# Kernel optimization log

Measured on AMD Instinct MI355X. Metric: run time of the kernel, lower is better.

The kernel has to match this reference:

```python
import jax, jax.numpy as jnp
import numpy as np

D, NH, DH, DM = 1024, 16, 64, 4096
B, S = 2, 2048
EPS = 1e-5


def _layernorm(x, w, b):
    mu = jnp.mean(x, axis=-1, keepdims=True)
    var = jnp.mean((x - mu) ** 2, axis=-1, keepdims=True)
    return (x - mu) * jax.lax.rsqrt(var + EPS) * w + b


def setup_inputs() -> dict:
    key = jax.random.key(0)
    ks = jax.random.split(key, 8)
    scale = D ** (-0.5)
    x = jax.random.normal(ks[0], (B, S, D), dtype=jnp.float32)
    WQ = jax.random.normal(ks[1], (NH, D, DH), dtype=jnp.float32) * scale
    WK = jax.random.normal(ks[2], (NH, D, DH), dtype=jnp.float32) * scale
    WV = jax.random.normal(ks[3], (NH, D, DH), dtype=jnp.float32) * scale
    WO = jax.random.normal(ks[4], (NH, DH, D), dtype=jnp.float32) * scale
    # MLP: torch Linear default init ~ U(-1/sqrt(fan_in), 1/sqrt(fan_in)); stored as [in, out]
    W1 = jax.random.uniform(ks[5], (D, DM), dtype=jnp.float32, minval=-1.0, maxval=1.0) * D ** (-0.5)
    b1 = jnp.zeros((DM,), dtype=jnp.float32)
    W2 = jax.random.uniform(ks[6], (DM, D), dtype=jnp.float32, minval=-1.0, maxval=1.0) * DM ** (-0.5)
    b2 = jnp.zeros((D,), dtype=jnp.float32)
    ln1_w = jnp.ones((D,), dtype=jnp.float32)
    ln1_b = jnp.zeros((D,), dtype=jnp.float32)
    ln2_w = jnp.ones((D,), dtype=jnp.float32)
    ln2_b = jnp.zeros((D,), dtype=jnp.float32)
    return {"x": x, "WQ": WQ, "WK": WK, "WV": WV, "WO": WO,
            "W1": W1, "b1": b1, "W2": W2, "b2": b2,
            "ln1_w": ln1_w, "ln1_b": ln1_b, "ln2_w": ln2_w, "ln2_b": ln2_b}


def reference(x, WQ, WK, WV, WO, W1, b1, W2, b2, ln1_w, ln1_b, ln2_w, ln2_b):
    s = x.shape[1]
    dh = WQ.shape[-1]
    r = x
    h = _layernorm(x, ln1_w, ln1_b)
    # batched across all heads (original loops over h; math identical)
    Q = jnp.einsum('bsd,hde->bhse', h, WQ)
    K = jnp.einsum('bsd,hde->bhse', h, WK)
    V = jnp.einsum('bsd,hde->bhse', h, WV)
    scores = jnp.einsum('bhqe,bhke->bhqk', Q, K) / jnp.sqrt(jnp.float32(dh))
    causal = jnp.tril(jnp.ones((s, s), dtype=bool))  # True = keep
    scores = jnp.where(causal, scores, -jnp.inf)
    attn = jax.nn.softmax(scores, axis=-1)
    ctx = jnp.einsum('bhqk,bhke->bhqe', attn, V)
    ao = jnp.einsum('bhqe,hed->bqd', ctx, WO)  # sum over heads
    x = r + ao
    h2 = _layernorm(x, ln2_w, ln2_b)
    mlp = jax.nn.gelu(h2 @ W1 + b1, approximate=False) @ W2 + b2
    return x + mlp
```

## Files before the change

### kernel.cpp

```cpp
#include <hip/hip_runtime.h>
#include <hip/hip_bf16.h>
#include <cstdint>

#define D_MODEL 1024
#define NHEADS 16
#define DHEAD 64
#define DMLP 4096
#define BATCH 2
#define SEQ 2048
#define ROWS (BATCH*SEQ)
#define LN_EPS 1e-5f

typedef __attribute__((ext_vector_type(8))) short short8;
typedef __attribute__((ext_vector_type(4))) float f32x4;

typedef const __attribute__((address_space(1))) uint32_t* gas_ptr;
typedef __attribute__((address_space(3))) uint32_t* las_ptr;

__device__ __forceinline__ short f2bf(float f) {
  union { float f; uint32_t u; } v; v.f = f;
  uint32_t r = v.u + 0x7FFFu + ((v.u >> 16) & 1u);
  return (short)(r >> 16);
}
__device__ __forceinline__ float bf2f(short s) {
  union { uint32_t u; float f; } v; v.u = ((uint32_t)(uint16_t)s) << 16;
  return v.f;
}

__global__ void ln_kernel(const float* __restrict__ x, const float* __restrict__ w,
                          const float* __restrict__ b, short* __restrict__ out) {
  int row = blockIdx.x;
  int t = threadIdx.x;
  const float4 v = ((const float4*)(x + (size_t)row * D_MODEL))[t];
  float s = v.x + v.y + v.z + v.w;
  float s2 = v.x*v.x + v.y*v.y + v.z*v.z + v.w*v.w;
#pragma unroll
  for (int k = 1; k < 64; k <<= 1) { s += __shfl_xor(s, k); s2 += __shfl_xor(s2, k); }
  __shared__ float red[8];
  int wv = t >> 6;
  if ((t & 63) == 0) { red[wv] = s; red[wv + 4] = s2; }
  __syncthreads();
  s = red[0] + red[1] + red[2] + red[3];
  s2 = red[4] + red[5] + red[6] + red[7];
  float mu = s * (1.0f / D_MODEL);
  float var = s2 * (1.0f / D_MODEL) - mu * mu;
  float rstd = rsqrtf(var + LN_EPS);
  const float4 wv4 = ((const float4*)w)[t];
  const float4 bv4 = ((const float4*)b)[t];
  short4 o4;
  o4.x = f2bf((v.x - mu) * rstd * wv4.x + bv4.x);
  o4.y = f2bf((v.y - mu) * rstd * wv4.y + bv4.y);
  o4.z = f2bf((v.z - mu) * rstd * wv4.z + bv4.z);
  o4.w = f2bf((v.w - mu) * rstd * wv4.w + bv4.w);
  *(short4*)(out + (size_t)row * D_MODEL + t * 4) = o4;
}

__global__ void reduce_ln(float* __restrict__ out, const float* __restrict__ part,
                          const float* __restrict__ w, const float* __restrict__ b,
                          short* __restrict__ h2) {
  int row = blockIdx.x;
  int t = threadIdx.x;
  float4 v = ((float4*)(out + (size_t)row * D_MODEL))[t];
  const float4 q = ((const float4*)(part + (size_t)row * D_MODEL))[t];
  v.x += q.x; v.y += q.y; v.z += q.z; v.w += q.w;
  ((float4*)(out + (size_t)row * D_MODEL))[t] = v;
  float s = v.x + v.y + v.z + v.w;
  float s2 = v.x*v.x + v.y*v.y + v.z*v.z + v.w*v.w;
#pragma unroll
  for (int k = 1; k < 64; k <<= 1) { s += __shfl_xor(s, k); s2 += __shfl_xor(s2, k); }
  __shared__ float red[8];
  int wv = t >> 6;
  if ((t & 63) == 0) { red[wv] = s; red[wv + 4] = s2; }
  __syncthreads();
  s = red[0] + red[1] + red[2] + red[3];
  s2 = red[4] + red[5] + red[6] + red[7];
  float mu = s * (1.0f / D_MODEL);
  float var = s2 * (1.0f / D_MODEL) - mu * mu;
  float rstd = rsqrtf(var + LN_EPS);
  const float4 wv4 = ((const float4*)w)[t];
  const float4 bv4 = ((const float4*)b)[t];
  short4 o4;
  o4.x = f2bf((v.x - mu) * rstd * wv4.x + bv4.x);
  o4.y = f2bf((v.y - mu) * rstd * wv4.y + bv4.y);
  o4.z = f2bf((v.z - mu) * rstd * wv4.z + bv4.z);
  o4.w = f2bf((v.w - mu) * rstd * wv4.w + bv4.w);
  *(short4*)(h2 + (size_t)row * D_MODEL + t * 4) = o4;
}

__global__ __launch_bounds__(256) void transpose_tile(const float* __restrict__ src, short* __restrict__ dst,
                                                      int R, int C, int srcMatStride) {
  __shared__ float tile[64][65];
  const int m = blockIdx.z;
  const int r0 = blockIdx.y * 64, c0 = blockIdx.x * 64;
  const int tx = threadIdx.x & 15, ty = threadIdx.x >> 4;
  const float* s = src + (size_t)m * srcMatStride + (size_t)r0 * C + c0;
#pragma unroll
  for (int i = 0; i < 4; i++) {
    float4 v = *(const float4*)(s + (size_t)(ty + i * 16) * C + tx * 4);
    tile[ty + i * 16][tx * 4 + 0] = v.x;
    tile[ty + i * 16][tx * 4 + 1] = v.y;
    tile[ty + i * 16][tx * 4 + 2] = v.z;
    tile[ty + i * 16][tx * 4 + 3] = v.w;
  }
  __syncthreads();
  short* d = dst + (size_t)m * C * R + (size_t)c0 * R + r0;
#pragma unroll
  for (int p = 0; p < 4; p++) {
    int c = ty + p * 16;
    int r4 = tx * 4;
    short4 o;
    o.x = f2bf(tile[r4 + 0][c]);
    o.y = f2bf(tile[r4 + 1][c]);
    o.z = f2bf(tile[r4 + 2][c]);
    o.w = f2bf(tile[r4 + 3][c]);
    *(short4*)(d + (size_t)c * R + r4) = o;
  }
}

template<int EPI>
__global__ __launch_bounds__(256) void gemm_bt(const short* __restrict__ A, const short* __restrict__ BT,
    const float* __restrict__ bias, const float* __restrict__ resid,
    float* __restrict__ outf, short* __restrict__ outb, float* __restrict__ part,
    int M, int N, int K, int LDA, int LDB) {
  __shared__ alignas(16) short As[2][8192];
  __shared__ alignas(16) short Bs[2][8192];
  const int t = threadIdx.x;
  const int l = t & 63, w = t >> 6;
  const int l15 = l & 15, l4 = l >> 4;

  const int nx = gridDim.x;
  const int sw = nx >> 3;
  int dd = blockIdx.y * nx + blockIdx.x;
  const int xcd = dd & 7, li = dd >> 3;
  const int bx = xcd * sw + (li % sw);
  const int by = li / sw;
  const int row0 = by * 128, col0 = bx * 128;

  if (EPI == 5) {
    A  += (size_t)blockIdx.z * K;
    BT += (size_t)blockIdx.z * K;
  }
  f32x4 acc[4][4] = {};

  char* AsB = (char*)As;
  char* BsB = (char*)Bs;

  auto stg = [&](int ti) {
    const int bo = (ti & 1) * 16384;
    const int k0 = ti << 6;
#pragma unroll
    for (int i = 0; i < 4; i++) {
      const int g = (i * 4 + w) * 64 + l;
      const int gr = g >> 3, sp = g & 7;
      const int co = k0 + ((sp ^ (gr & 7)) << 3);
      __builtin_amdgcn_global_load_lds((gas_ptr)(A  + (size_t)(row0 + gr) * LDA + co),
                                       (las_ptr)(AsB + bo + g * 16), 16, 0, 0);
      __builtin_amdgcn_global_load_lds((gas_ptr)(BT + (size_t)(col0 + gr) * LDB + co),
                                       (las_ptr)(BsB + bo + g * 16), 16, 0, 0);
    }
  };

  const int nk = K >> 6;
  stg(0);
  asm volatile("s_waitcnt vmcnt(0)" ::: "memory");
  __builtin_amdgcn_s_barrier();

  const int wr = (w >> 1) * 64, wc = (w & 1) * 64;

  for (int ti = 0; ti < nk; ti++) {
    const int bo = (ti & 1) * 16384;
    if (ti + 1 < nk) stg(ti + 1);
#pragma unroll
    for (int kg = 0; kg < 2; kg++) {
      const int sl = ((kg * 4 + l4) ^ (l15 & 7)) * 16;
      short8 a[4], bfr[4];
#pragma unroll
      for (int m = 0; m < 4; m++) a[m]   = *(const short8*)(AsB + bo + (wr + m * 16 + l15) * 128 + sl);
#pragma unroll
      for (int n = 0; n < 4; n++) bfr[n] = *(const short8*)(BsB + bo + (wc + n * 16 + l15) * 128 + sl);
#pragma unroll
      for (int m = 0; m < 4; m++)
#pragma unroll
        for (int n = 0; n < 4; n++)
          acc[m][n] = __builtin_amdgcn_mfma_f32_16x16x32_bf16(a[m], bfr[n], acc[m][n], 0, 0, 0);
    }
    if (ti + 1 < nk) { asm volatile("s_waitcnt vmcnt(0)" ::: "memory"); }
    __builtin_amdgcn_s_barrier();
  }

#pragma unroll
  for (int m = 0; m < 4; m++) {
#pragma unroll
    for (int n = 0; n < 4; n++) {
#pragma unroll
      for (int j = 0; j < 4; j++) {
        int R_ = row0 + wr + m * 16 + l4 * 4 + j;
        int C_ = col0 + wc + n * 16 + l15;
        float v = acc[m][n][j];
        size_t o = (size_t)R_ * N + C_;
        if (EPI == 0) {
          outb[o] = f2bf(v);
        } else if (EPI == 2) {
          float xx = v + bias[C_];
          outb[o] = f2bf(0.5f * xx * (1.0f + erff(xx * 0.70710678118f)));
        } else if (EPI == 5) {
          if (blockIdx.z == 0) outf[o] = v + (bias ? bias[C_] : 0.0f) + resid[o];
          else part[o] = v;
        }
      }
    }
  }
}

__global__ void reduce1(float* __restrict__ out, const float* __restrict__ p, int n4) {
  for (int i = blockIdx.x * 256 + threadIdx.x; i < n4; i += gridDim.x * 256) {
    float4 o = ((float4*)out)[i];
    float4 q = ((const float4*)p)[i];
    o.x += q.x; o.y += q.y; o.z += q.z; o.w += q.w;
    ((float4*)out)[i] = o;
  }
}

__device__ __forceinline__ void attn_step(
    int kt_, int qt, int bufP,
    const short* __restrict__ base, const short* __restrict__ vbase,
    short8& vWA, short8& vWB,
    short8& vLA, short8& vLB,
    const short8 qf[2],
    char* KsB, char* VtB, char* PlB,
    f32x4 acc[4], float mrun[4], float lrun[4],
    int w, int l, int q0, int vr, int vd0)
{
  const int l15 = l & 15, l4 = l >> 4;
  const int bufQ = bufP ^ 1;
  if (kt_ < qt) {
#pragma unroll
    for (int i = 0; i < 8; i++) {
      int d = vd0 + i;
      int cs = (vr >> 2) ^ ((d >> 3) & 7);
      uint32_t val = (uint32_t)(uint16_t)vWA[i] | ((uint32_t)(uint16_t)vWB[i] << 16);
      *(uint32_t*)(VtB + bufQ * 9216 + d * 144 + cs * 16 + (vr & 3) * 4) = val;
    }
#pragma unroll
    for (int i = 0; i < 2; i++) {
      int g = (w * 2 + i) * 64 + l;
      int key = g >> 3, ck = g & 7;
      const short* src = base + (size_t)((kt_ + 1) * 64 + key) * 3072 + 1024 + ((ck ^ (key & 7)) * 8);
      __builtin_amdgcn_global_load_lds((gas_ptr)src, (las_ptr)(KsB + bufQ * 8192 + g * 16), 16, 0, 0);
    }
  }
  if (kt_ + 2 <= qt) {
    vLA = *(const short8*)(vbase + (size_t)((kt_ + 2) * 64 + 2 * vr) * 3072);
    vLB = *(const short8*)(vbase + (size_t)((kt_ + 2) * 64 + 2 * vr + 1) * 3072);
  }

  f32x4 sc[4];
#pragma unroll
  for (int cb = 0; cb < 4; cb++) {
    f32x4 s = {};
    int key = cb * 16 + l15;
#pragma unroll
    for (int c = 0; c < 2; c++) {
      int ck = (c * 4 + l4) ^ (key & 7);
      short8 kf = *(const short8*)(KsB + bufP * 8192 + key * 128 + ck * 16);
      s = __builtin_amdgcn_mfma_f32_16x16x32_bf16(qf[c], kf, s, 0, 0, 0);
    }
    sc[cb] = s;
  }

  const bool lastt = (kt_ == qt);
  float alpha[4];
#pragma unroll
  for (int jj = 0; jj < 4; jj++) {
    int qg = q0 + l4 * 4 + jj;
    float s0 = sc[0][jj] * 0.125f;
    float s1 = sc[1][jj] * 0.125f;
    float s2 = sc[2][jj] * 0.125f;
    float s3 = sc[3][jj] * 0.125f;
    if (lastt) {
      int kg = kt_ * 64 + l15;
      if (kg      > qg) s0 = -1e30f;
      if (kg + 16 > qg) s1 = -1e30f;
      if (kg + 32 > qg) s2 = -1e30f;
      if (kg + 48 > qg) s3 = -1e30f;
    }
    float rm = fmaxf(fmaxf(s0, s1), fmaxf(s2, s3));
    rm = fmaxf(rm, __shfl_xor(rm, 1));
    rm = fmaxf(rm, __shfl_xor(rm, 2));
    rm = fmaxf(rm, __shfl_xor(rm, 4));
    rm = fmaxf(rm, __shfl_xor(rm, 8));
    float nm = fmaxf(mrun[jj], rm);
    float al = __expf(mrun[jj] - nm);
    mrun[jj] = nm;
    float p0 = __expf(s0 - nm), p1 = __expf(s1 - nm);
    float p2 = __expf(s2 - nm), p3 = __expf(s3 - nm);
    float ps = p0 + p1 + p2 + p3;
    ps += __shfl_xor(ps, 1);
    ps += __shfl_xor(ps, 2);
    ps += __shfl_xor(ps, 4);
    ps += __shfl_xor(ps, 8);
    lrun[jj] = lrun[jj] * al + ps;
    alpha[jj] = al;
    short* pr = (short*)(PlB + (l4 * 4 + jj) * 144);
    pr[l15]      = f2bf(p0);
    pr[16 + l15] = f2bf(p1);
    pr[32 + l15] = f2bf(p2);
    pr[48 + l15] = f2bf(p3);
  }
#pragma unroll
  for (int db = 0; db < 4; db++) {
    f32x4 a = acc[db];
    a[0] *= alpha[0]; a[1] *= alpha[1]; a[2] *= alpha[2]; a[3] *= alpha[3];
    acc[db] = a;
  }
#pragma unroll
  for (int kc = 0; kc < 2; kc++) {
    short8 pf = *(const short8*)(PlB + l15 * 144 + kc * 64 + l4 * 16);
#pragma unroll
    for (int db = 0; db < 4; db++) {
      int d = db * 16 + l15;
      int cs = (kc * 4 + l4) ^ ((d >> 3) & 7);
      short8 vf = *(const short8*)(VtB + bufP * 9216 + d * 144 + cs * 16);
      acc[db] = __builtin_amdgcn_mfma_f32_16x16x32_bf16(pf, vf, acc[db], 0, 0, 0);
    }
  }
}

__global__ __launch_bounds__(256) void attn_mfma(const short* __restrict__ qkv, short* __restrict__ ctx) {
  __shared__ alignas(16) short Ks[2 * 64 * 64];
  __shared__ alignas(16) short Vt[2 * 64 * 72];
  __shared__ alignas(16) short Pl[4][16 * 72];
  const int t = threadIdx.x;
  const int l = t & 63;
  const int w = t >> 6;
  const int l15 = l & 15, l4 = l >> 4;
  const int bh = blockIdx.x;
  const int b = bh >> 4, h = bh & 15;
  const int qt = (gridDim.y - 1) - blockIdx.y;
  const int q0 = qt * 64 + w * 16;

  const short* base = qkv + (size_t)b * SEQ * 3072 + h * 64;

  short8 qf[2];
#pragma unroll
  for (int c = 0; c < 2; c++)
    qf[c] = *(const short8*)(base + (size_t)(q0 + l15) * 3072 + c * 32 + l4 * 8);

  const int vr = t >> 3;
  const int vd0 = (t & 7) * 8;
  const short* vbase = base + 2048 + vd0;

  char* KsB = (char*)Ks;
  char* VtB = (char*)Vt;
  char* PlB = (char*)&Pl[w][0];

  short8 va0, vb0, va1, vb1;
  va0 = *(const short8*)(vbase + (size_t)(2 * vr) * 3072);
  vb0 = *(const short8*)(vbase + (size_t)(2 * vr + 1) * 3072);
  if (qt >= 1) {
    va1 = *(const short8*)(vbase + (size_t)(64 + 2 * vr) * 3072);
    vb1 = *(const short8*)(vbase + (size_t)(64 + 2 * vr + 1) * 3072);
  }
#pragma unroll
  for (int i = 0; i < 8; i++) {
    int d = vd0 + i;
    int cs = (vr >> 2) ^ ((d >> 3) & 7);
    uint32_t val = (uint32_t)(uint16_t)va0[i] | ((uint32_t)(uint16_t)vb0[i] << 16);
    *(uint32_t*)(VtB + d * 144 + cs * 16 + (vr & 3) * 4) = val;
  }
#pragma unroll
  for (int i = 0; i < 2; i++) {
    int g = (w * 2 + i) * 64 + l;
    int key = g >> 3, ck = g & 7;
    const short* src = base + (size_t)key * 3072 + 1024 + ((ck ^ (key & 7)) * 8);
    __builtin_amdgcn_global_load_lds((gas_ptr)src, (las_ptr)(KsB + g * 16), 16, 0, 0);
  }
  __syncthreads();

  f32x4 acc[4] = {};
  float mrun[4] = {-1e30f, -1e30f, -1e30f, -1e30f};
  float lrun[4] = {0.f, 0.f, 0.f, 0.f};

  int kt = 0;
  while (true) {
    attn_step(kt, qt, 0, base, vbase, va1, vb1, va0, vb0, qf,
              KsB, VtB, PlB, acc, mrun, lrun, w, l, q0, vr, vd0);
    __syncthreads();
    if (++kt > qt) break;
    attn_step(kt, qt, 1, base, vbase, va0, vb0, va1, vb1, qf,
              KsB, VtB, PlB, acc, mrun, lrun, w, l, q0, vr, vd0);
    __syncthreads();
    if (++kt > qt) break;
  }

  float inv[4];
#pragma unroll
  for (int jj = 0; jj < 4; jj++) inv[jj] = 1.0f / lrun[jj];
  short* obase = ctx + (size_t)(b * SEQ + q0) * D_MODEL + h * 64;
#pragma unroll
  for (int db = 0; db < 4; db++)
#pragma unroll
    for (int jj = 0; jj < 4; jj++)
      obase[(size_t)(l4 * 4 + jj) * D_MODEL + db * 16 + l15] = f2bf(acc[db][jj] * inv[jj]);
}

extern "C" void kernel_launch(void* const* d_in, const int* in_sizes, int n_in,
                              void* d_out, int out_size, void* d_ws, size_t ws_size,
                              hipStream_t stream) {
  (void)in_sizes; (void)n_in; (void)out_size; (void)ws_size;
  const float* x    = (const float*)d_in[0];
  const float* WQ   = (const float*)d_in[1];
  const float* WK   = (const float*)d_in[2];
  const float* WV   = (const float*)d_in[3];
  const float* WO   = (const float*)d_in[4];
  const float* W1   = (const float*)d_in[5];
  const float* b1   = (const float*)d_in[6];
  const float* W2   = (const float*)d_in[7];
  const float* b2   = (const float*)d_in[8];
  const float* ln1w = (const float*)d_in[9];
  const float* ln1b = (const float*)d_in[10];
  const float* ln2w = (const float*)d_in[11];
  const float* ln2b = (const float*)d_in[12];
  float* out = (float*)d_out;

  char* p = (char*)d_ws;
  short* h1    = (short*)p; p += (size_t)ROWS * D_MODEL * 2;
  short* ctx   = (short*)p; p += (size_t)ROWS * D_MODEL * 2;
  short* h2    = (short*)p; p += (size_t)ROWS * D_MODEL * 2;
  short* m1    = (short*)p; p += (size_t)ROWS * DMLP * 2;
  short* wqkvT = (short*)p; p += (size_t)3 * D_MODEL * D_MODEL * 2;
  short* woT   = (short*)p; p += (size_t)D_MODEL * D_MODEL * 2;
  short* w1T   = (short*)p; p += (size_t)D_MODEL * DMLP * 2;
  short* w2T   = (short*)p; p += (size_t)D_MODEL * DMLP * 2;
  short* qkv   = (short*)p; p += (size_t)ROWS * 3 * D_MODEL * 2;

  float* fp1 = (float*)qkv;

  transpose_tile<<<dim3(1, 16, 16), 256, 0, stream>>>(WQ, wqkvT,                   1024, 64, D_MODEL * DHEAD);
  transpose_tile<<<dim3(1, 16, 16), 256, 0, stream>>>(WK, wqkvT + 1024 * 1024,     1024, 64, D_MODEL * DHEAD);
  transpose_tile<<<dim3(1, 16, 16), 256, 0, stream>>>(WV, wqkvT + 2 * 1024 * 1024, 1024, 64, D_MODEL * DHEAD);
  transpose_tile<<<dim3(16, 16, 1), 256, 0, stream>>>(WO, woT, 1024, 1024, 0);
  transpose_tile<<<dim3(64, 16, 1), 256, 0, stream>>>(W1, w1T, 1024, 4096, 0);
  transpose_tile<<<dim3(16, 64, 1), 256, 0, stream>>>(W2, w2T, 4096, 1024, 0);

  ln_kernel<<<ROWS, 256, 0, stream>>>(x, ln1w, ln1b, h1);
  gemm_bt<0><<<dim3(3 * D_MODEL / 128, ROWS / 128), 256, 0, stream>>>(
      h1, wqkvT, nullptr, nullptr, nullptr, qkv, nullptr,
      ROWS, 3 * D_MODEL, D_MODEL, D_MODEL, D_MODEL);
  attn_mfma<<<dim3(BATCH * NHEADS, SEQ / 64), 256, 0, stream>>>(qkv, ctx);
  gemm_bt<5><<<dim3(D_MODEL / 128, ROWS / 128, 2), 256, 0, stream>>>(
      ctx, woT, nullptr, x, out, nullptr, fp1,
      ROWS, D_MODEL, D_MODEL / 2, D_MODEL, D_MODEL);
  reduce_ln<<<ROWS, 256, 0, stream>>>(out, fp1, ln2w, ln2b, h2);
  gemm_bt<2><<<dim3(DMLP / 128, ROWS / 128), 256, 0, stream>>>(
      h2, w1T, b1, nullptr, nullptr, m1, nullptr,
      ROWS, DMLP, D_MODEL, D_MODEL, D_MODEL);
  gemm_bt<5><<<dim3(D_MODEL / 128, ROWS / 128, 2), 256, 0, stream>>>(
      m1, w2T, b2, out, out, nullptr, fp1,
      ROWS, D_MODEL, DMLP / 2, DMLP, DMLP);
  reduce1<<<2048, 256, 0, stream>>>(out, fp1, ROWS * D_MODEL / 4);
}
```

Baseline: 298.0 us.

## Pre-pack weights into swizzled tile-contiguous panels for GEMM B loads

```diff
diff --git a/kernel.cpp b/kernel.cpp
--- a/kernel.cpp
+++ b/kernel.cpp
@@ -87,41 +87,34 @@
   *(short4*)(h2 + (size_t)row * D_MODEL + t * 4) = o4;
 }
 
-__global__ __launch_bounds__(256) void transpose_tile(const float* __restrict__ src, short* __restrict__ dst,
-                                                      int R, int C, int srcMatStride) {
-  __shared__ float tile[64][65];
-  const int m = blockIdx.z;
-  const int r0 = blockIdx.y * 64, c0 = blockIdx.x * 64;
-  const int tx = threadIdx.x & 15, ty = threadIdx.x >> 4;
-  const float* s = src + (size_t)m * srcMatStride + (size_t)r0 * C + c0;
-#pragma unroll
-  for (int i = 0; i < 4; i++) {
-    float4 v = *(const float4*)(s + (size_t)(ty + i * 16) * C + tx * 4);
-    tile[ty + i * 16][tx * 4 + 0] = v.x;
-    tile[ty + i * 16][tx * 4 + 1] = v.y;
-    tile[ty + i * 16][tx * 4 + 2] = v.z;
-    tile[ty + i * 16][tx * 4 + 3] = v.w;
-  }
-  __syncthreads();
-  short* d = dst + (size_t)m * C * R + (size_t)c0 * R + r0;
-#pragma unroll
-  for (int p = 0; p < 4; p++) {
-    int c = ty + p * 16;
-    int r4 = tx * 4;
-    short4 o;
-    o.x = f2bf(tile[r4 + 0][c]);
-    o.y = f2bf(tile[r4 + 1][c]);
-    o.z = f2bf(tile[r4 + 2][c]);
-    o.w = f2bf(tile[r4 + 3][c]);
-    *(short4*)(d + (size_t)c * R + r4) = o;
+__global__ __launch_bounds__(256) void repack_w(const float* __restrict__ W, short* __restrict__ out,
+                                                int nkt, int ks1, int ks2, int ns1, int ns2) {
+  const int cp = blockIdx.x, kt = blockIdx.y;
+  const int t = threadIdx.x;
+  const int cc = t & 127;
+  const int kh = t >> 7;
+  const int n = cp * 128 + cc;
+  const int nbase = (n >> 6) * ns1 + (n & 63) * ns2;
+  short* dst = out + (((size_t)cp * nkt + kt) * 128 + cc) * 64;
+#pragma unroll
+  for (int ci = 0; ci < 4; ci++) {
+    const int c = kh * 4 + ci;
+    short8 ch;
+#pragma unroll
+    for (int j = 0; j < 8; j++) {
+      int k = kt * 64 + c * 8 + j;
+      ch[j] = f2bf(W[(k >> 6) * ks1 + (k & 63) * ks2 + nbase]);
+    }
+    const int sp = c ^ (cc & 7);
+    *(short8*)(dst + sp * 8) = ch;
   }
 }
 
 template<int EPI>
-__global__ __launch_bounds__(256) void gemm_bt(const short* __restrict__ A, const short* __restrict__ BT,
+__global__ __launch_bounds__(256) void gemm_bt(const short* __restrict__ A, const short* __restrict__ Bpk,
     const float* __restrict__ bias, const float* __restrict__ resid,
     float* __restrict__ outf, short* __restrict__ outb, float* __restrict__ part,
-    int M, int N, int K, int LDA, int LDB) {
+    int M, int N, int K, int LDA, int KFULL) {
   __shared__ alignas(16) short As[2][8192];
   __shared__ alignas(16) short Bs[2][8192];
   const int t = threadIdx.x;
@@ -136,10 +129,14 @@
   const int by = li / sw;
   const int row0 = by * 128, col0 = bx * 128;
 
+  const int NKT = KFULL >> 6;
+  int ktB = 0;
   if (EPI == 5) {
     A  += (size_t)blockIdx.z * K;
-    BT += (size_t)blockIdx.z * K;
-  }
+    ktB = blockIdx.z * (K >> 6);
+  }
+  const short* Bpan = Bpk + (size_t)bx * NKT * 8192;
+
   f32x4 acc[4][4] = {};
 
   char* AsB = (char*)As;
@@ -148,14 +145,15 @@
   auto stg = [&](int ti) {
     const int bo = (ti & 1) * 16384;
     const int k0 = ti << 6;
+    const short* bsrc = Bpan + (size_t)(ktB + ti) * 8192;
 #pragma unroll
     for (int i = 0; i < 4; i++) {
-      const int g = (i * 4 + w) * 64 + l;
+      const int g = i * 256 + t;
       const int gr = g >> 3, sp = g & 7;
       const int co = k0 + ((sp ^ (gr & 7)) << 3);
-      __builtin_amdgcn_global_load_lds((gas_ptr)(A  + (size_t)(row0 + gr) * LDA + co),
+      __builtin_amdgcn_global_load_lds((gas_ptr)(A + (size_t)(row0 + gr) * LDA + co),
                                        (las_ptr)(AsB + bo + g * 16), 16, 0, 0);
-      __builtin_amdgcn_global_load_lds((gas_ptr)(BT + (size_t)(col0 + gr) * LDB + co),
+      __builtin_amdgcn_global_load_lds((gas_ptr)(bsrc + (size_t)g * 8),
                                        (las_ptr)(BsB + bo + g * 16), 16, 0, 0);
     }
   };
@@ -436,12 +434,12 @@
 
   float* fp1 = (float*)qkv;
 
-  transpose_tile<<<dim3(1, 16, 16), 256, 0, stream>>>(WQ, wqkvT,                   1024, 64, D_MODEL * DHEAD);
-  transpose_tile<<<dim3(1, 16, 16), 256, 0, stream>>>(WK, wqkvT + 1024 * 1024,     1024, 64, D_MODEL * DHEAD);
-  transpose_tile<<<dim3(1, 16, 16), 256, 0, stream>>>(WV, wqkvT + 2 * 1024 * 1024, 1024, 64, D_MODEL * DHEAD);
-  transpose_tile<<<dim3(16, 16, 1), 256, 0, stream>>>(WO, woT, 1024, 1024, 0);
-  transpose_tile<<<dim3(64, 16, 1), 256, 0, stream>>>(W1, w1T, 1024, 4096, 0);
-  transpose_tile<<<dim3(16, 64, 1), 256, 0, stream>>>(W2, w2T, 4096, 1024, 0);
+  repack_w<<<dim3(8, 16), 256, 0, stream>>>(WQ, wqkvT,                 16, 4096, 64, 65536, 1);
+  repack_w<<<dim3(8, 16), 256, 0, stream>>>(WK, wqkvT + 8 * 16 * 8192, 16, 4096, 64, 65536, 1);
+  repack_w<<<dim3(8, 16), 256, 0, stream>>>(WV, wqkvT + 16 * 16 * 8192, 16, 4096, 64, 65536, 1);
+  repack_w<<<dim3(8, 16), 256, 0, stream>>>(WO, woT, 16, 65536, 1024, 64, 1);
+  repack_w<<<dim3(32, 16), 256, 0, stream>>>(W1, w1T, 16, 262144, 4096, 64, 1);
+  repack_w<<<dim3(8, 64), 256, 0, stream>>>(W2, w2T, 64, 65536, 1024, 64, 1);
 
   ln_kernel<<<ROWS, 256, 0, stream>>>(x, ln1w, ln1b, h1);
   gemm_bt<0><<<dim3(3 * D_MODEL / 128, ROWS / 128), 256, 0, stream>>>(
```

New measurement: 299.9 us. Within noise of the previous version (+0.7%).
